# Optimization experiments

Measured on AMD Instinct MI355X. Metric: run time of the kernel, lower is better.

The kernel has to match this reference:

```python
import jax, jax.numpy as jnp
import numpy as np
import math

N_HEADS = 8

def setup_inputs() -> dict:
    key = jax.random.key(0)
    qkv = jax.random.normal(key, (4, 1536, 2048), dtype=jnp.float32)
    return {"qkv": qkv}

def reference(qkv):
    bs, width, length = qkv.shape
    ch = width // (3 * N_HEADS)
    # reshape to [bs*n_heads, 3*ch, length] then split into q, k, v
    qkv_h = qkv.reshape(bs * N_HEADS, 3 * ch, length)
    q = qkv_h[:, :ch]
    k = qkv_h[:, ch:2 * ch]
    v = qkv_h[:, 2 * ch:]
    scale = 1.0 / math.sqrt(math.sqrt(ch))
    # scores: [B*H, T, S]
    weight = jnp.einsum('bct,bcs->bts', q * scale, k * scale)
    weight = jax.nn.softmax(weight.astype(jnp.float32), axis=-1).astype(weight.dtype)
    a = jnp.einsum('bts,bcs->bct', weight, v)  # [B*H, ch, T]
    return a.reshape(bs, N_HEADS * ch, length)
```

## Files before the change

kernel.cpp:

```cpp
#include <hip/hip_runtime.h>
#include <hip/hip_bf16.h>

typedef __attribute__((ext_vector_type(8))) short bf16x8;
typedef __attribute__((ext_vector_type(8))) unsigned short u16x8;
typedef __attribute__((ext_vector_type(4))) float f32x4;

#define SEQ 2048
#define BT 128
#define BS 64
#define NBH 32
#define QSCALE 0.1803368801111204f

#if __has_builtin(__builtin_amdgcn_exp2f)
#define EXP2(x) __builtin_amdgcn_exp2f(x)
#else
#define EXP2(x) exp2f(x)
#endif

__device__ __forceinline__ unsigned short bfc(float f) {
  union { __hip_bfloat16 h; unsigned short u; } v;
  v.h = __float2bfloat16(f);
  return v.u;
}

__device__ __forceinline__ void gl_lds16(const void* g, void* l) {
  __builtin_amdgcn_global_load_lds((__attribute__((address_space(1))) void*)g,
                                   (__attribute__((address_space(3))) void*)l, 16, 0, 0);
}

__global__ __launch_bounds__(256)
void prep_kernel(const float* __restrict__ qkv, unsigned short* __restrict__ ws) {
  const int tid = threadIdx.x;
  const int b = blockIdx.x;
  if (b < 4096) {
    int gid = b * 256 + tid;
    int sec = gid >> 19;
    int r = gid & 524287;
    int bh = r >> 14;
    int rr = r & 16383;
    int cc = rr >> 11;
    int t = rr & 2047;
    const float* src = qkv + ((size_t)(bh >> 3) * 1536 + (bh & 7) * 192 + sec * 64 + cc * 8) * SEQ + t;
    const float scale = sec ? 1.0f : QSCALE;
    u16x8 o;
    #pragma unroll
    for (int e = 0; e < 8; ++e) o[e] = bfc(src[(size_t)e * SEQ] * scale);
    unsigned short* dst = ws + ((size_t)sec * NBH * SEQ + (size_t)bh * SEQ + t) * 64;
    *(u16x8*)(dst + ((cc ^ (t & 7)) * 8)) = o;
  } else {
    int cid = (b - 4096) * 256 + tid;
    int bh = cid >> 14;
    int rr = cid & 16383;
    int c = rr >> 8;
    int cc = rr & 255;
    int grp = cc >> 3, sub = cc & 7;
    const float* src = qkv + ((size_t)(bh >> 3) * 1536 + (bh & 7) * 192 + 128 + c) * SEQ + cc * 8;
    float4 a = *(const float4*)(src);
    float4 bv = *(const float4*)(src + 4);
    u16x8 o;
    o[0] = bfc(a.x); o[1] = bfc(a.y); o[2] = bfc(a.z); o[3] = bfc(a.w);
    o[4] = bfc(bv.x); o[5] = bfc(bv.y); o[6] = bfc(bv.z); o[7] = bfc(bv.w);
    unsigned short* dst = ws + (size_t)2 * NBH * SEQ * 64 +
                          ((size_t)bh * 64 + c) * SEQ + grp * 64 + ((sub ^ (c & 7)) * 8);
    *(u16x8*)dst = o;
  }
}

__global__ __launch_bounds__(512, 4)
void attn_main(const unsigned short* __restrict__ ws, float* __restrict__ out) {
  const int bid = blockIdx.x;
  const int bh = (bid & 7) + 8 * ((bid >> 3) >> 4);
  const int tile = (bid >> 3) & 15;
  const int t0 = tile * BT;

  const unsigned short* Qws = ws + ((size_t)bh * SEQ + t0) * 64;
  const unsigned short* Kws = ws + (size_t)NBH * SEQ * 64 + (size_t)bh * SEQ * 64;
  const unsigned short* Vws = ws + (size_t)2 * NBH * SEQ * 64 + (size_t)bh * 64 * SEQ;
  float* __restrict__ outb = out + (size_t)bh * 64 * SEQ;

  __shared__ __align__(16) unsigned short QP[BT * 64];
  __shared__ __align__(16) unsigned short Kt[2][BS * 64];
  __shared__ __align__(16) unsigned short Vt[2][BS * 64];

  const int tid = threadIdx.x;
  const int w = tid >> 6;
  const int l = tid & 63;
  const int lr = l & 15;
  const int g = l >> 4;
  const int sw = lr & 7;
  const int prow = (w * 16 + lr) * 64;

  const int srow = tid >> 3, scc = tid & 7;
  const unsigned short* kg = Kws + (size_t)srow * 64 + scc * 8;
  const unsigned short* vg = Vws + (size_t)srow * SEQ + scc * 8;

  gl_lds16(Qws + (size_t)srow * 64 + scc * 8, &QP[tid * 8]);
  gl_lds16(Qws + (size_t)(64 + srow) * 64 + scc * 8, &QP[4096 + tid * 8]);
  gl_lds16(kg, &Kt[0][tid * 8]);
  gl_lds16(vg, &Vt[0][tid * 8]);
  __syncthreads();

  bf16x8 qB0 = *(const bf16x8*)&QP[prow + ((g ^ sw) * 8)];
  bf16x8 qB1 = *(const bf16x8*)&QP[prow + (((g + 4) ^ sw) * 8)];

  const f32x4 fz = (f32x4){0.f, 0.f, 0.f, 0.f};
  bf16x8 onesB;
  #pragma unroll
  for (int i = 0; i < 8; ++i) onesB[i] = (short)0x3F80;

  f32x4 pv[4];
  #pragma unroll
  for (int i = 0; i < 4; ++i) pv[i] = fz;
  f32x4 psum = fz;

  int cur = 0;
  for (int it = 0; it < SEQ / BS; ++it) {
    const int s1 = ((it + 1) & 31) * BS;
    gl_lds16(kg + (size_t)s1 * 64, &Kt[cur ^ 1][tid * 8]);
    gl_lds16(vg + s1, &Vt[cur ^ 1][tid * 8]);

    const unsigned short* kb = Kt[cur];
    const unsigned short* vb = Vt[cur];

    f32x4 acc[4];
    #pragma unroll
    for (int ch = 0; ch < 2; ++ch) {
      bf16x8 qb = ch ? qB1 : qB0;
      #pragma unroll
      for (int sub = 0; sub < 4; ++sub) {
        bf16x8 ka = *(const bf16x8*)&kb[(sub * 16 + lr) * 64 + (((g + 4 * ch) ^ sw) * 8)];
        acc[sub] = __builtin_amdgcn_mfma_f32_16x16x32_bf16(ka, qb, ch ? acc[sub] : fz, 0, 0, 0);
      }
    }

    #pragma unroll
    for (int sub = 0; sub < 4; ++sub) {
      #pragma unroll
      for (int r = 0; r < 4; ++r) acc[sub][r] = EXP2(acc[sub][r]);
    }

    #pragma unroll
    for (int sub = 0; sub < 4; ++sub) {
      ushort4 pw = { bfc(acc[sub][0]), bfc(acc[sub][1]), bfc(acc[sub][2]), bfc(acc[sub][3]) };
      *(ushort4*)&QP[prow + (((2 * sub + (g >> 1)) ^ sw) * 8) + (g & 1) * 4] = pw;
    }
    bf16x8 pA0 = *(const bf16x8*)&QP[prow + ((g ^ sw) * 8)];
    bf16x8 pA1 = *(const bf16x8*)&QP[prow + (((4 + g) ^ sw) * 8)];

    psum = __builtin_amdgcn_mfma_f32_16x16x32_bf16(pA0, onesB, psum, 0, 0, 0);
    psum = __builtin_amdgcn_mfma_f32_16x16x32_bf16(pA1, onesB, psum, 0, 0, 0);

    #pragma unroll
    for (int cs = 0; cs < 4; ++cs) {
      bf16x8 v0 = *(const bf16x8*)&vb[(cs * 16 + lr) * 64 + ((g ^ sw) * 8)];
      bf16x8 v1 = *(const bf16x8*)&vb[(cs * 16 + lr) * 64 + (((g + 4) ^ sw) * 8)];
      pv[cs] = __builtin_amdgcn_mfma_f32_16x16x32_bf16(pA0, v0, pv[cs], 0, 0, 0);
      pv[cs] = __builtin_amdgcn_mfma_f32_16x16x32_bf16(pA1, v1, pv[cs], 0, 0, 0);
    }

    __syncthreads();
    cur ^= 1;
  }

  {
    float linv[4];
    #pragma unroll
    for (int r = 0; r < 4; ++r) linv[r] = 1.0f / psum[r];
    #pragma unroll
    for (int cs = 0; cs < 4; ++cs) {
      #pragma unroll
      for (int r = 0; r < 4; ++r) {
        outb[(cs * 16 + lr) * SEQ + t0 + w * 16 + g * 4 + r] = pv[cs][r] * linv[r];
      }
    }
  }
}

#define PAD 72
__device__ __forceinline__ unsigned short f2bf(float f) {
  union { float f; unsigned u; } v; v.f = f;
  return (unsigned short)((v.u + 0x7fffu + ((v.u >> 16) & 1u)) >> 16);
}

__global__ __launch_bounds__(512, 4)
void qkv_attn_fallback(const float* __restrict__ qkv, float* __restrict__ out) {
  const int bid = blockIdx.x;
  const int xcd = bid & 7;
  const int slot = bid >> 3;
  const int bh = xcd + 8 * (slot >> 4);
  const int tile = slot & 15;
  const int t0 = tile * BT;

  const float* __restrict__ base = qkv + (size_t)((bh >> 3) * 1536 + (bh & 7) * 192) * SEQ;
  const float* __restrict__ qg = base;
  const float* __restrict__ kg = base + 64 * SEQ;
  const float* __restrict__ vg = base + 128 * SEQ;
  float* __restrict__ outb = out + (size_t)bh * 64 * SEQ;

  __shared__ __align__(16) unsigned short Qt[BT * PAD];
  __shared__ __align__(16) unsigned short Kt[BS * PAD];
  __shared__ __align__(16) unsigned short Vt[64 * PAD];
  __shared__ __align__(16) unsigned short Pl[BT * PAD];

  const int tid = threadIdx.x;
  const int w = tid >> 6;
  const int l = tid & 63;
  const int lr = l & 15;
  const int g = l >> 4;

  {
    const int cb = tid >> 5, tb = tid & 31;
    const int c0 = cb * 4, tt0 = tb * 4;
    const float* p = qg + c0 * SEQ + t0 + tt0;
    float4 r0 = *(const float4*)(p);
    float4 r1 = *(const float4*)(p + SEQ);
    float4 r2 = *(const float4*)(p + 2 * SEQ);
    float4 r3 = *(const float4*)(p + 3 * SEQ);
    const float s = 0.125f;
    ushort4 w0 = { f2bf(r0.x*s), f2bf(r1.x*s), f2bf(r2.x*s), f2bf(r3.x*s) };
    ushort4 w1 = { f2bf(r0.y*s), f2bf(r1.y*s), f2bf(r2.y*s), f2bf(r3.y*s) };
    ushort4 w2 = { f2bf(r0.z*s), f2bf(r1.z*s), f2bf(r2.z*s), f2bf(r3.z*s) };
    ushort4 w3 = { f2bf(r0.w*s), f2bf(r1.w*s), f2bf(r2.w*s), f2bf(r3.w*s) };
    *(ushort4*)&Qt[(tt0 + 0) * PAD + c0] = w0;
    *(ushort4*)&Qt[(tt0 + 1) * PAD + c0] = w1;
    *(ushort4*)&Qt[(tt0 + 2) * PAD + c0] = w2;
    *(ushort4*)&Qt[(tt0 + 3) * PAD + c0] = w3;
  }
  __syncthreads();

  bf16x8 qB0 = *(const bf16x8*)&Qt[(w * 16 + lr) * PAD + g * 8];
  bf16x8 qB1 = *(const bf16x8*)&Qt[(w * 16 + lr) * PAD + g * 8 + 32];

  f32x4 pv[4];
  #pragma unroll
  for (int i = 0; i < 4; ++i) pv[i] = (f32x4){0.f, 0.f, 0.f, 0.f};
  float mrun = -1e30f;
  float lsum = 0.f;

  for (int s0 = 0; s0 < SEQ; s0 += BS) {
    __syncthreads();
    {
      const int cb = tid >> 4, sb = tid & 15;
      const int c0 = cb * 2, sl = sb * 4;
      const float* p0 = kg + c0 * SEQ + s0 + sl;
      float4 a0 = *(const float4*)(p0);
      float4 a1 = *(const float4*)(p0 + SEQ);
      ushort2 y0 = { f2bf(a0.x), f2bf(a1.x) };
      ushort2 y1 = { f2bf(a0.y), f2bf(a1.y) };
      ushort2 y2 = { f2bf(a0.z), f2bf(a1.z) };
      ushort2 y3 = { f2bf(a0.w), f2bf(a1.w) };
      *(ushort2*)&Kt[(sl + 0) * PAD + c0] = y0;
      *(ushort2*)&Kt[(sl + 1) * PAD + c0] = y1;
      *(ushort2*)&Kt[(sl + 2) * PAD + c0] = y2;
      *(ushort2*)&Kt[(sl + 3) * PAD + c0] = y3;
    }
    {
      const int c = tid >> 3;
      const int sq = (tid & 7) * 8;
      const float* p0 = vg + c * SEQ + s0 + sq;
      float4 b0 = *(const float4*)(p0);
      float4 b1 = *(const float4*)(p0 + 4);
      ushort4 z0 = { f2bf(b0.x), f2bf(b0.y), f2bf(b0.z), f2bf(b0.w) };
      ushort4 z1 = { f2bf(b1.x), f2bf(b1.y), f2bf(b1.z), f2bf(b1.w) };
      *(ushort4*)&Vt[c * PAD + sq] = z0;
      *(ushort4*)&Vt[c * PAD + sq + 4] = z1;
    }
    __syncthreads();

    f32x4 acc[4];
    #pragma unroll
    for (int i = 0; i < 4; ++i) acc[i] = (f32x4){0.f, 0.f, 0.f, 0.f};
    #pragma unroll
    for (int ch = 0; ch < 2; ++ch) {
      bf16x8 qb = ch ? qB1 : qB0;
      #pragma unroll
      for (int sub = 0; sub < 4; ++sub) {
        bf16x8 ka = *(const bf16x8*)&Kt[(sub * 16 + lr) * PAD + g * 8 + 32 * ch];
        acc[sub] = __builtin_amdgcn_mfma_f32_16x16x32_bf16(ka, qb, acc[sub], 0, 0, 0);
      }
    }

    float pmax = -1e30f;
    #pragma unroll
    for (int sub = 0; sub < 4; ++sub)
      #pragma unroll
      for (int r = 0; r < 4; ++r) pmax = fmaxf(pmax, acc[sub][r]);
    pmax = fmaxf(pmax, __shfl_xor(pmax, 16));
    pmax = fmaxf(pmax, __shfl_xor(pmax, 32));
    const float mnew = fmaxf(mrun, pmax);
    const float alpha = __expf(mrun - mnew);
    float rsum = 0.f;
    #pragma unroll
    for (int sub = 0; sub < 4; ++sub) {
      #pragma unroll
      for (int r = 0; r < 4; ++r) {
        float p = __expf(acc[sub][r] - mnew);
        acc[sub][r] = p;
        rsum += p;
      }
    }
    rsum += __shfl_xor(rsum, 16);
    rsum += __shfl_xor(rsum, 32);
    lsum = lsum * alpha + rsum;
    mrun = mnew;

    #pragma unroll
    for (int sub = 0; sub < 4; ++sub) {
      ushort4 pw = { f2bf(acc[sub][0]), f2bf(acc[sub][1]), f2bf(acc[sub][2]), f2bf(acc[sub][3]) };
      *(ushort4*)&Pl[(w * 16 + lr) * PAD + sub * 16 + g * 4] = pw;
    }

    {
      const int sbase = (l & 48) + g * 4;
      #pragma unroll
      for (int r = 0; r < 4; ++r) {
        float ar = __shfl(alpha, sbase + r, 64);
        #pragma unroll
        for (int cs = 0; cs < 4; ++cs) pv[cs][r] *= ar;
      }
    }

    bf16x8 pA0 = *(const bf16x8*)&Pl[(w * 16 + lr) * PAD + g * 8];
    bf16x8 pA1 = *(const bf16x8*)&Pl[(w * 16 + lr) * PAD + g * 8 + 32];
    #pragma unroll
    for (int cs = 0; cs < 4; ++cs) {
      bf16x8 v0 = *(const bf16x8*)&Vt[(cs * 16 + lr) * PAD + g * 8];
      bf16x8 v1 = *(const bf16x8*)&Vt[(cs * 16 + lr) * PAD + g * 8 + 32];
      pv[cs] = __builtin_amdgcn_mfma_f32_16x16x32_bf16(pA0, v0, pv[cs], 0, 0, 0);
      pv[cs] = __builtin_amdgcn_mfma_f32_16x16x32_bf16(pA1, v1, pv[cs], 0, 0, 0);
    }
  }

  {
    const int sbase = (l & 48) + g * 4;
    float linv[4];
    #pragma unroll
    for (int r = 0; r < 4; ++r) linv[r] = 1.0f / __shfl(lsum, sbase + r, 64);
    #pragma unroll
    for (int cs = 0; cs < 4; ++cs) {
      #pragma unroll
      for (int r = 0; r < 4; ++r) {
        outb[(cs * 16 + lr) * SEQ + t0 + w * 16 + g * 4 + r] = pv[cs][r] * linv[r];
      }
    }
  }
}

extern "C" void kernel_launch(void* const* d_in, const int* in_sizes, int n_in,
                              void* d_out, int out_size, void* d_ws, size_t ws_size,
                              hipStream_t stream) {
  const float* qkv = (const float*)d_in[0];
  float* out = (float*)d_out;
  const size_t need = (size_t)3 * NBH * SEQ * 64 * sizeof(unsigned short);
  if (ws_size >= need) {
    unsigned short* ws = (unsigned short*)d_ws;
    prep_kernel<<<dim3(6144), dim3(256), 0, stream>>>(qkv, ws);
    attn_main<<<dim3(512), dim3(512), 0, stream>>>(ws, out);
  } else {
    qkv_attn_fallback<<<dim3(512), dim3(512), 0, stream>>>(qkv, out);
  }
}
```

Before: 67.72 us.

## Switch attention to 32x32x16 MFMA with register-resident P via permlane swaps

Rewrites the main attention kernel to use 4 waves of 256 threads, each handling 32 query rows with 32x32x16 bf16 MFMAs instead of 16x16x32. The softmax probabilities are packed with v_cvt_pk_bf16_f32 and rearranged into A-operand layout with v_permlane32_swap, so they no longer round-trip through LDS. Larger MFMA tiles raise operand reuse per LDS read. The cost is higher register pressure from 16-wide accumulators and fewer threads per block, which reduces parallelism for latency hiding.

Result: faster. 66.25 us (-2.2%).

```diff
diff --git a/kernel.cpp b/kernel.cpp
--- a/kernel.cpp
+++ b/kernel.cpp
@@ -4,6 +4,7 @@
 typedef __attribute__((ext_vector_type(8))) short bf16x8;
 typedef __attribute__((ext_vector_type(8))) unsigned short u16x8;
 typedef __attribute__((ext_vector_type(4))) float f32x4;
+typedef __attribute__((ext_vector_type(16))) float f32x16;
 
 #define SEQ 2048
 #define BT 128
@@ -66,7 +67,7 @@
   }
 }
 
-__global__ __launch_bounds__(512, 4)
+__global__ __launch_bounds__(256, 2)
 void attn_main(const unsigned short* __restrict__ ws, float* __restrict__ out) {
   const int bid = blockIdx.x;
   const int bh = (bid & 7) + 8 * ((bid >> 3) >> 4);
@@ -85,77 +86,96 @@
   const int tid = threadIdx.x;
   const int w = tid >> 6;
   const int l = tid & 63;
-  const int lr = l & 15;
-  const int g = l >> 4;
-  const int sw = lr & 7;
-  const int prow = (w * 16 + lr) * 64;
-
-  const int srow = tid >> 3, scc = tid & 7;
-  const unsigned short* kg = Kws + (size_t)srow * 64 + scc * 8;
-  const unsigned short* vg = Vws + (size_t)srow * SEQ + scc * 8;
-
-  gl_lds16(Qws + (size_t)srow * 64 + scc * 8, &QP[tid * 8]);
-  gl_lds16(Qws + (size_t)(64 + srow) * 64 + scc * 8, &QP[4096 + tid * 8]);
-  gl_lds16(kg, &Kt[0][tid * 8]);
-  gl_lds16(vg, &Vt[0][tid * 8]);
+  const int lw = l & 31;
+  const int h = l >> 5;
+  const int sw = lw & 7;
+
+  #pragma unroll
+  for (int i = 0; i < 4; ++i)
+    gl_lds16(Qws + (size_t)(tid + i * 256) * 8, &QP[(tid + i * 256) * 8]);
+  gl_lds16(Kws + (size_t)tid * 8, &Kt[0][tid * 8]);
+  gl_lds16(Kws + (size_t)(tid + 256) * 8, &Kt[0][(tid + 256) * 8]);
+  gl_lds16(Vws + (size_t)(tid >> 3) * SEQ + (tid & 7) * 8, &Vt[0][tid * 8]);
+  gl_lds16(Vws + (size_t)((tid >> 3) + 32) * SEQ + (tid & 7) * 8, &Vt[0][(tid + 256) * 8]);
   __syncthreads();
 
-  bf16x8 qB0 = *(const bf16x8*)&QP[prow + ((g ^ sw) * 8)];
-  bf16x8 qB1 = *(const bf16x8*)&QP[prow + (((g + 4) ^ sw) * 8)];
-
-  const f32x4 fz = (f32x4){0.f, 0.f, 0.f, 0.f};
+  bf16x8 qB[4];
+  {
+    const int rloc = w * 32 + lw;
+    #pragma unroll
+    for (int kc = 0; kc < 4; ++kc)
+      qB[kc] = *(const bf16x8*)&QP[rloc * 64 + (((2 * kc + h) ^ sw) * 8)];
+  }
+
+  f32x16 zero16;
+  #pragma unroll
+  for (int i = 0; i < 16; ++i) zero16[i] = 0.f;
   bf16x8 onesB;
   #pragma unroll
   for (int i = 0; i < 8; ++i) onesB[i] = (short)0x3F80;
 
-  f32x4 pv[4];
-  #pragma unroll
-  for (int i = 0; i < 4; ++i) pv[i] = fz;
-  f32x4 psum = fz;
+  f32x16 accO[2]; f32x16 psum;
+  accO[0] = zero16; accO[1] = zero16; psum = zero16;
 
   int cur = 0;
+  #pragma unroll 1
   for (int it = 0; it < SEQ / BS; ++it) {
-    const int s1 = ((it + 1) & 31) * BS;
-    gl_lds16(kg + (size_t)s1 * 64, &Kt[cur ^ 1][tid * 8]);
-    gl_lds16(vg + s1, &Vt[cur ^ 1][tid * 8]);
+    const int s1 = (it + 1) & 31;
+    gl_lds16(Kws + (size_t)s1 * 4096 + tid * 8, &Kt[cur ^ 1][tid * 8]);
+    gl_lds16(Kws + (size_t)s1 * 4096 + (tid + 256) * 8, &Kt[cur ^ 1][(tid + 256) * 8]);
+    gl_lds16(Vws + (size_t)(tid >> 3) * SEQ + s1 * 64 + (tid & 7) * 8, &Vt[cur ^ 1][tid * 8]);
+    gl_lds16(Vws + (size_t)((tid >> 3) + 32) * SEQ + s1 * 64 + (tid & 7) * 8, &Vt[cur ^ 1][(tid + 256) * 8]);
 
     const unsigned short* kb = Kt[cur];
     const unsigned short* vb = Vt[cur];
 
-    f32x4 acc[4];
+    f32x16 accS[2];
+    #pragma unroll
+    for (int ms = 0; ms < 2; ++ms) {
+      #pragma unroll
+      for (int kc = 0; kc < 4; ++kc) {
+        bf16x8 ka = *(const bf16x8*)&kb[(32 * ms + lw) * 64 + (((2 * kc + h) ^ sw) * 8)];
+        accS[ms] = __builtin_amdgcn_mfma_f32_32x32x16_bf16(ka, qB[kc], kc ? accS[ms] : zero16, 0, 0, 0);
+      }
+    }
+
+    #pragma unroll
+    for (int ms = 0; ms < 2; ++ms)
+      #pragma unroll
+      for (int r = 0; r < 16; ++r) accS[ms][r] = EXP2(accS[ms][r]);
+
+    unsigned int pk[2][8];
+    #pragma unroll
+    for (int ms = 0; ms < 2; ++ms)
+      #pragma unroll
+      for (int wd = 0; wd < 8; ++wd)
+        asm("v_cvt_pk_bf16_f32 %0, %1, %2"
+            : "=v"(pk[ms][wd]) : "v"(accS[ms][2 * wd]), "v"(accS[ms][2 * wd + 1]));
+
+    bf16x8 pA[4];
+    #pragma unroll
+    for (int ks = 0; ks < 4; ++ks) {
+      const int a = ks & 1, ms = ks >> 1;
+      unsigned int x0 = pk[ms][4 * a + 0], y0 = pk[ms][4 * a + 2];
+      unsigned int x1 = pk[ms][4 * a + 1], y1 = pk[ms][4 * a + 3];
+      asm("v_permlane32_swap_b32 %0, %1" : "+v"(x0), "+v"(y0));
+      asm("v_permlane32_swap_b32 %0, %1" : "+v"(x1), "+v"(y1));
+      union { unsigned int u[4]; bf16x8 v; } uu;
+      uu.u[0] = x0; uu.u[1] = x1; uu.u[2] = y0; uu.u[3] = y1;
+      pA[ks] = uu.v;
+    }
+
+    #pragma unroll
+    for (int ks = 0; ks < 4; ++ks)
+      psum = __builtin_amdgcn_mfma_f32_32x32x16_bf16(pA[ks], onesB, psum, 0, 0, 0);
+
     #pragma unroll
     for (int ch = 0; ch < 2; ++ch) {
-      bf16x8 qb = ch ? qB1 : qB0;
-      #pragma unroll
-      for (int sub = 0; sub < 4; ++sub) {
-        bf16x8 ka = *(const bf16x8*)&kb[(sub * 16 + lr) * 64 + (((g + 4 * ch) ^ sw) * 8)];
-        acc[sub] = __builtin_amdgcn_mfma_f32_16x16x32_bf16(ka, qb, ch ? acc[sub] : fz, 0, 0, 0);
-      }
-    }
-
-    #pragma unroll
-    for (int sub = 0; sub < 4; ++sub) {
-      #pragma unroll
-      for (int r = 0; r < 4; ++r) acc[sub][r] = EXP2(acc[sub][r]);
-    }
-
-    #pragma unroll
-    for (int sub = 0; sub < 4; ++sub) {
-      ushort4 pw = { bfc(acc[sub][0]), bfc(acc[sub][1]), bfc(acc[sub][2]), bfc(acc[sub][3]) };
-      *(ushort4*)&QP[prow + (((2 * sub + (g >> 1)) ^ sw) * 8) + (g & 1) * 4] = pw;
-    }
-    bf16x8 pA0 = *(const bf16x8*)&QP[prow + ((g ^ sw) * 8)];
-    bf16x8 pA1 = *(const bf16x8*)&QP[prow + (((4 + g) ^ sw) * 8)];
-
-    psum = __builtin_amdgcn_mfma_f32_16x16x32_bf16(pA0, onesB, psum, 0, 0, 0);
-    psum = __builtin_amdgcn_mfma_f32_16x16x32_bf16(pA1, onesB, psum, 0, 0, 0);
-
-    #pragma unroll
-    for (int cs = 0; cs < 4; ++cs) {
-      bf16x8 v0 = *(const bf16x8*)&vb[(cs * 16 + lr) * 64 + ((g ^ sw) * 8)];
-      bf16x8 v1 = *(const bf16x8*)&vb[(cs * 16 + lr) * 64 + (((g + 4) ^ sw) * 8)];
-      pv[cs] = __builtin_amdgcn_mfma_f32_16x16x32_bf16(pA0, v0, pv[cs], 0, 0, 0);
-      pv[cs] = __builtin_amdgcn_mfma_f32_16x16x32_bf16(pA1, v1, pv[cs], 0, 0, 0);
+      #pragma unroll
+      for (int ks = 0; ks < 4; ++ks) {
+        bf16x8 vB = *(const bf16x8*)&vb[(32 * ch + lw) * 64 + (((2 * ks + h) ^ sw) * 8)];
+        accO[ch] = __builtin_amdgcn_mfma_f32_32x32x16_bf16(pA[ks], vB, accO[ch], 0, 0, 0);
+      }
     }
 
     __syncthreads();
@@ -163,14 +183,15 @@
   }
 
   {
-    float linv[4];
-    #pragma unroll
-    for (int r = 0; r < 4; ++r) linv[r] = 1.0f / psum[r];
-    #pragma unroll
-    for (int cs = 0; cs < 4; ++cs) {
-      #pragma unroll
-      for (int r = 0; r < 4; ++r) {
-        outb[(cs * 16 + lr) * SEQ + t0 + w * 16 + g * 4 + r] = pv[cs][r] * linv[r];
+    float linv[16];
+    #pragma unroll
+    for (int r = 0; r < 16; ++r) linv[r] = 1.0f / psum[r];
+    #pragma unroll
+    for (int ch = 0; ch < 2; ++ch) {
+      #pragma unroll
+      for (int r = 0; r < 16; ++r) {
+        const int tg = t0 + w * 32 + (r & 3) + 8 * (r >> 2) + 4 * h;
+        outb[(size_t)(32 * ch + lw) * SEQ + tg] = accO[ch][r] * linv[r];
       }
     }
   }
@@ -355,7 +376,7 @@
   if (ws_size >= need) {
     unsigned short* ws = (unsigned short*)d_ws;
     prep_kernel<<<dim3(6144), dim3(256), 0, stream>>>(qkv, ws);
-    attn_main<<<dim3(512), dim3(512), 0, stream>>>(ws, out);
+    attn_main<<<dim3(512), dim3(256), 0, stream>>>(ws, out);
   } else {
     qkv_attn_fallback<<<dim3(512), dim3(512), 0, stream>>>(qkv, out);
   }
```
